# Optimization experiments

Hardware: AMD Instinct MI355X
Metric: run time of the kernel (lower is better)

The kernel has to match this reference:

```python
import jax, jax.numpy as jnp
import numpy as np

NX, NY, NZ = 432, 496, 1
D = 64        # num_pt_features
K = 3         # NUM_K
M = 1024      # memory size
BEV = 128     # num_bev_features
NCOORD = 3
NV = 10000    # pillars in scene
NP = 16384    # points in scene
BN_EPS = 1e-3
SHRINK = 0.0025


def hard_shrink_relu(x, lambd, eps=1e-12):
    return jax.nn.relu(x - lambd) * x / (jnp.abs(x - lambd) + eps)


def batchnorm_train(x, gamma, beta, eps=BN_EPS):
    # torch BatchNorm1d training-mode math (biased variance)
    mu = jnp.mean(x, axis=0)
    var = jnp.mean((x - mu) ** 2, axis=0)
    return (x - mu) * jax.lax.rsqrt(var + eps) * gamma + beta


def pdist2(a, b, eps=1e-5):
    # sqrt(eps + |  ||a||^2 + ||b||^2 - 2 a.b |), shape [n1, n2]
    n1 = jnp.sum(a * a, axis=1, keepdims=True)
    n2 = jnp.sum(b * b, axis=1, keepdims=True)
    d2 = n1 + n2.T - 2.0 * (a @ b.T)
    return jnp.sqrt(eps + jnp.abs(d2))


def memory_lookup(x_flat, mem_w, shrink):
    # MemAE-style memory unit: softmax addressing + hard shrink + L1 renorm
    att = jax.nn.softmax(x_flat @ mem_w.T, axis=1)          # [N, M]
    att = hard_shrink_relu(att, shrink)
    att = att / jnp.maximum(jnp.sum(jnp.abs(att), axis=1, keepdims=True), 1e-12)
    return att @ mem_w                                       # [N, D]


def setup_inputs() -> dict:
    key = jax.random.key(0)
    ks = jax.random.split(key, 8)
    rng = np.random.default_rng(0)
    flat = rng.choice(NX * NY, size=NV, replace=False)       # unique BEV cells
    x = (flat % NX).astype(np.int32)
    y = (flat // NX).astype(np.int32)
    coords = jnp.asarray(np.stack([np.zeros(NV, np.int32), x, y,
                                   np.zeros(NV, np.int32)], axis=1))  # (b, x, y, z)
    pc = jax.random.uniform(ks[1], (NP, 4), dtype=jnp.float32)
    point_coords = pc * jnp.array([0.0, NX, NY, 1.0], dtype=jnp.float32)
    return {
        "pillar_features": jax.random.normal(ks[0], (NV, D), dtype=jnp.float32),
        "coords": coords,
        "point_features": jax.random.normal(ks[2], (NP, D), dtype=jnp.float32),
        "point_coords": point_coords,
        "adapt_w": jax.random.normal(ks[3], (BEV // 2, D * K), dtype=jnp.float32) * 0.05,
        "bn1_g": jnp.ones((BEV // 2,), dtype=jnp.float32),
        "bn1_b": jnp.zeros((BEV // 2,), dtype=jnp.float32),
        "weight_w": jax.random.normal(ks[4], (2, BEV // 2), dtype=jnp.float32) * 0.1,
        "bn2_g": jnp.ones((2,), dtype=jnp.float32),
        "bn2_b": jnp.zeros((2,), dtype=jnp.float32),
        "mem_w": jax.random.normal(ks[5], (M, D), dtype=jnp.float32) * 0.1,
    }


def reference(pillar_features, coords, point_features, point_coords,
              adapt_w, bn1_g, bn1_b, weight_w, bn2_g, bn2_b, mem_w):
    nv = pillar_features.shape[0]
    pillars = pillar_features.T                              # [D, nv]

    # --- coord-based retrieval: smallest-K pdist(pillar coords, point coords) ---
    dist = pdist2(coords.astype(jnp.float32), point_coords)  # [nv, np]
    _, idx_c = jax.lax.top_k(-dist, K)                       # [nv, K]
    pillars_positive_coord = point_features[idx_c]           # [nv, K, D]

    # --- feature-based retrieval: top-K of softmax(points @ pillars, axis=0) ---
    score = jax.nn.softmax(point_features @ pillars, axis=0) # [np, nv]
    _, idx_f = jax.lax.top_k(score.T, K)                     # [nv, K]
    points_positive = point_features[idx_f]                  # [nv, K, D]

    # --- memory unit on both branches ---
    out_f = memory_lookup(points_positive.reshape(nv * K, D), mem_w, SHRINK).reshape(nv, K * D)
    out_c = memory_lookup(pillars_positive_coord.reshape(nv * K, D), mem_w, SHRINK).reshape(nv, K * D)

    f = jax.nn.relu(batchnorm_train(out_f @ adapt_w.T, bn1_g, bn1_b))  # [nv, 64]
    c = jax.nn.relu(batchnorm_train(out_c @ adapt_w.T, bn1_g, bn1_b))  # [nv, 64]
    w = jax.nn.softmax(batchnorm_train(pillar_features @ weight_w.T, bn2_g, bn2_b), axis=-1)
    pillars_aug = w[:, :1] * f + w[:, 1:2] * c               # [nv, 64]
    pillars_full = jnp.concatenate([pillars, pillars_aug.T], axis=0)  # [128, nv]

    # --- scatter to BEV canvas ---
    bev_idx = coords[:, 1] + coords[:, 2] * NX + coords[:, 3]
    spatial = jnp.zeros((BEV, NX * NY), dtype=pillar_features.dtype).at[:, bev_idx].set(pillars_full)
    pind = jnp.zeros((NCOORD, NX * NY), dtype=pillar_features.dtype)
    pind = pind.at[0, bev_idx].set(coords[:, 2].astype(jnp.float32))
    pind = pind.at[1, bev_idx].set(coords[:, 3].astype(jnp.float32))
    pind = pind.at[2, bev_idx].set(coords[:, 1].astype(jnp.float32))

    spatial_features = spatial.reshape(1, BEV * NZ, NY, NX)
    spatial_indices = pind.reshape(1, NCOORD * NZ, NY, NX)
    return spatial_features, spatial_indices
```

## Files before the change

### kernel.cpp

```cpp
#include <hip/hip_runtime.h>
#include <math.h>

#define NXc 432
#define NYc 496
#define NVc 10000
#define NPc 16384
#define CELLS (NXc*NYc)
#define SHRINKc 0.0025f
#define NVPAD 10048
#define NBX 27
#define NBY 31
#define NBIN (NBX*NBY)

typedef unsigned short u16;
typedef __attribute__((ext_vector_type(8))) short s16x8;
typedef __attribute__((ext_vector_type(4))) float f32x4;

__global__ void k_zero(float* __restrict__ out, int n, float* __restrict__ stats,
                       int* __restrict__ binCnt) {
    int gid = blockIdx.x * blockDim.x + threadIdx.x;
    int n4 = n >> 2;
    float4 z = make_float4(0.f, 0.f, 0.f, 0.f);
    float4* o4 = (float4*)out;
    for (int i = gid; i < n4; i += gridDim.x * blockDim.x) o4[i] = z;
    int tail = n & 3;
    if (gid < tail) out[n4 * 4 + gid] = 0.f;
    if (gid < 260) stats[gid] = 0.f;
    if (gid >= 512 && gid < 512 + NBIN) binCnt[gid - 512] = 0;
}

__device__ __forceinline__ u16 f2b(float x) {
    unsigned u = __float_as_uint(x);
    unsigned r = (u + 0x7fffu + ((u >> 16) & 1u)) >> 16;
    return (u16)r;
}
__global__ __launch_bounds__(256) void k_cast(const float* __restrict__ pillar,
                                              const float* __restrict__ pfeat,
                                              const float* __restrict__ memw,
                                              const float* __restrict__ pcoord,
                                              u16* __restrict__ pillarH,
                                              u16* __restrict__ pfeatH,
                                              u16* __restrict__ memwH,
                                              u16* __restrict__ memwTH,
                                              int* __restrict__ binCnt) {
    int idx = blockIdx.x * 256 + threadIdx.x;
    const int N1 = NVPAD * 64;
    const int N2 = N1 + NPc * 64;
    const int N3 = N2 + 65536;
    const int N4 = N3 + 65536;
    if (idx < N1) {
        int v = idx >> 6;
        pillarH[idx] = f2b(v < NVc ? pillar[idx] : 0.f);
    } else if (idx < N2) {
        int j = idx - N1;
        pfeatH[j] = f2b(pfeat[j]);
    } else if (idx < N3) {
        int j = idx - N2;
        memwH[j] = f2b(memw[j]);
    } else if (idx < N4) {
        int i = idx - N3;
        int d = i >> 10, j = i & 1023;
        memwTH[i] = f2b(memw[j * 64 + d]);
    } else {
        int j = idx - N4;
        float qx = pcoord[j * 4 + 1], qy = pcoord[j * 4 + 2];
        int bx = (int)(qx * 0.0625f); if (bx > NBX - 1) bx = NBX - 1;
        int by = (int)(qy * 0.0625f); if (by > NBY - 1) by = NBY - 1;
        atomicAdd(&binCnt[by * NBX + bx], 1);
    }
}

__global__ __launch_bounds__(1024) void k_binscan(const int* __restrict__ binCnt,
                                                  int* __restrict__ binStart,
                                                  int* __restrict__ binCursor) {
    __shared__ int sc[1024];
    int t = threadIdx.x;
    int vcount = (t < NBIN) ? binCnt[t] : 0;
    sc[t] = vcount;
    __syncthreads();
    for (int off = 1; off < 1024; off <<= 1) {
        int add = (t >= off) ? sc[t - off] : 0;
        __syncthreads();
        sc[t] += add;
        __syncthreads();
    }
    int excl = sc[t] - vcount;
    if (t <= NBIN) { binStart[t] = excl; binCursor[t] = excl; }
}

__global__ __launch_bounds__(256) void k_binfill(const float* __restrict__ pcoord,
                                                 int* __restrict__ binCursor,
                                                 float4* __restrict__ binPC) {
    int j = blockIdx.x * 256 + threadIdx.x;
    float qx = pcoord[j * 4 + 1], qy = pcoord[j * 4 + 2], qz = pcoord[j * 4 + 3];
    int bx = (int)(qx * 0.0625f); if (bx > NBX - 1) bx = NBX - 1;
    int by = (int)(qy * 0.0625f); if (by > NBY - 1) by = NBY - 1;
    int slot = atomicAdd(&binCursor[by * NBX + bx], 1);
    binPC[slot] = make_float4(qx, qy, qz * qz, __uint_as_float((unsigned)j));
}

__device__ __forceinline__ void ins_max4(unsigned &k0, unsigned &k1, unsigned &k2,
                                         unsigned &k3, unsigned t) {
    unsigned n;
    n = k0 > t ? k0 : t;  t = k0 > t ? t : k0;  k0 = n;
    n = k1 > t ? k1 : t;  t = k1 > t ? t : k1;  k1 = n;
    n = k2 > t ? k2 : t;  t = k2 > t ? t : k2;  k2 = n;
    k3 = k3 > t ? k3 : t;
}
__device__ __forceinline__ void ins_min4(unsigned &k0, unsigned &k1, unsigned &k2,
                                         unsigned &k3, unsigned t) {
    unsigned n;
    n = k0 < t ? k0 : t;  t = k0 < t ? t : k0;  k0 = n;
    n = k1 < t ? k1 : t;  t = k1 < t ? t : k1;  k1 = n;
    n = k2 < t ? k2 : t;  t = k2 < t ? t : k2;  k2 = n;
    k3 = k3 < t ? k3 : t;
}
__device__ __forceinline__ void ins_min6(unsigned kk[6], unsigned t) {
    unsigned n;
#pragma unroll
    for (int i = 0; i < 5; ++i) {
        n = kk[i] < t ? kk[i] : t;  t = kk[i] < t ? t : kk[i];  kk[i] = n;
    }
    kk[5] = kk[5] < t ? kk[5] : t;
}

__global__ __launch_bounds__(256) void k_dist6(const int* __restrict__ coords,
                                               const float4* __restrict__ binPC,
                                               const int* __restrict__ binStart,
                                               int* __restrict__ dIdx6) {
    int v = blockIdx.x * 256 + threadIdx.x;
    if (v >= NVc) return;
    int xi = coords[v * 4 + 1], yi = coords[v * 4 + 2];
    float x = (float)xi, y = (float)yi;
    int bx = xi >> 4; if (bx > NBX - 1) bx = NBX - 1;
    int by = yi >> 4; if (by > NBY - 1) by = NBY - 1;
    unsigned kk[6] = {~0u, ~0u, ~0u, ~0u, ~0u, ~0u};
    for (int r = 0; r < 32; ++r) {
        int x0 = bx - r, x1 = bx + r, y0 = by - r, y1 = by + r;
        for (int cy = y0; cy <= y1; ++cy) {
            if (cy < 0 || cy > NBY - 1) continue;
            int step = (cy == y0 || cy == y1) ? 1 : (x1 > x0 ? x1 - x0 : 1);
            for (int cx = x0; cx <= x1; cx += step) {
                if (cx < 0 || cx > NBX - 1) continue;
                int b = cy * NBX + cx;
                int s0 = binStart[b], s1 = binStart[b + 1];
                for (int s = s0; s < s1; ++s) {
                    float4 p = binPC[s];
                    float e1 = x - p.x, e2 = y - p.y;
                    float d2 = fmaf(e1, e1, fmaf(e2, e2, p.z));
                    unsigned key = (__float_as_uint(d2) & 0xFFFFC000u) | __float_as_uint(p.w);
                    ins_min6(kk, key);
                }
            }
        }
        if (kk[2] != ~0u) {
            float d3 = __uint_as_float(kk[2] & 0xFFFFC000u);
            if (256.f * (float)(r * r) > d3 * 1.004f + 1e-3f) break;
        }
    }
#pragma unroll
    for (int j = 0; j < 6; ++j) dIdx6[v * 6 + j] = (int)(kk[j] & 16383u);
}

__global__ __launch_bounds__(256) void k_score4(const u16* __restrict__ pillarH,
                                                const u16* __restrict__ pfeatH,
                                                int* __restrict__ sIdx) {
    __shared__ unsigned SH[4096];
    u16* BF = (u16*)SH;
    int t = threadIdx.x;
    int w = t >> 6, l = t & 63;
    int lm = l & 15, qd = l >> 4;
    int pb = blockIdx.x * 64;
    int cb = blockIdx.y * 1024;

    const u16* arow = pillarH + (size_t)(pb + 16 * w + lm) * 64 + qd * 8;
    s16x8 a0 = *(const s16x8*)arow;
    s16x8 a1 = *(const s16x8*)(arow + 32);

    unsigned sk[4][4];
#pragma unroll
    for (int r = 0; r < 4; ++r)
#pragma unroll
        for (int j = 0; j < 4; ++j) sk[r][j] = 0u;

    for (int s = 0; s < 8; ++s) {
        int ptb = cb + s * 128;
#pragma unroll
        for (int r = 0; r < 4; ++r) {
            int q = t + 256 * r;
            int row = q >> 3, g = q & 7;
            uint4 v = *(const uint4*)(pfeatH + (size_t)(ptb + row) * 64 + g * 8);
            *(uint4*)&BF[(((row >> 4) * 8 + g) * 16 + ((row & 15) ^ g)) * 8] = v;
        }
        __syncthreads();
#pragma unroll
        for (int pt = 0; pt < 8; ++pt) {
            s16x8 b0 = *(const s16x8*)&BF[(((pt * 8 + qd) * 16) + (lm ^ qd)) * 8];
            s16x8 b1 = *(const s16x8*)&BF[(((pt * 8 + qd + 4) * 16) + (lm ^ (qd + 4))) * 8];
            f32x4 acc = {256.f, 256.f, 256.f, 256.f};
            acc = __builtin_amdgcn_mfma_f32_16x16x32_bf16(a0, b0, acc, 0, 0, 0);
            acc = __builtin_amdgcn_mfma_f32_16x16x32_bf16(a1, b1, acc, 0, 0, 0);
            unsigned idf = (unsigned)(1023 - (s * 128 + pt * 16 + lm));
#pragma unroll
            for (int r = 0; r < 4; ++r) {
                unsigned key = (__float_as_uint(acc[r]) & 0xFFFFFC00u) | idf;
                ins_max4(sk[r][0], sk[r][1], sk[r][2], sk[r][3], key);
            }
        }
        __syncthreads();
    }
#pragma unroll
    for (int r = 0; r < 4; ++r) {
        int row = 16 * w + qd * 4 + r;
        *(uint4*)&SH[(row * 16 + lm) * 4] = make_uint4(sk[r][0], sk[r][1], sk[r][2], sk[r][3]);
    }
    __syncthreads();
    if (t < 64) {
        int gpr = pb + t;
        unsigned m0 = 0u, m1 = 0u, m2 = 0u, m3 = 0u;
#pragma unroll 4
        for (int cc = 0; cc < 16; ++cc) {
            uint4 v = *(const uint4*)&SH[(t * 16 + cc) * 4];
            ins_max4(m0, m1, m2, m3, v.x);
            ins_max4(m0, m1, m2, m3, v.y);
            ins_max4(m0, m1, m2, m3, v.z);
            ins_max4(m0, m1, m2, m3, v.w);
        }
        if (gpr < NVc) {
            int base = (blockIdx.y * NVc + gpr) * 4;
            sIdx[base + 0] = cb + 1023 - (int)(m0 & 1023u);
            sIdx[base + 1] = cb + 1023 - (int)(m1 & 1023u);
            sIdx[base + 2] = cb + 1023 - (int)(m2 & 1023u);
            sIdx[base + 3] = cb + 1023 - (int)(m3 & 1023u);
        }
    }
}

__global__ __launch_bounds__(256) void k_rerank(const float* __restrict__ pillar,
                                                const int* __restrict__ coords,
                                                const float* __restrict__ pfeat,
                                                const float* __restrict__ pcoord,
                                                const int* __restrict__ sIdx,
                                                const int* __restrict__ dIdx6,
                                                int* __restrict__ idx_f,
                                                int* __restrict__ idx_c) {
    int t = threadIdx.x;
    int wv = t >> 6, l = t & 63;
    int v = blockIdx.x * 4 + wv;
    int chunk = l >> 2, slot = l & 3;
    int ps = sIdx[(chunk * NVc + v) * 4 + slot];
    int pd = dIdx6[v * 6 + (l < 6 ? l : 0)];
    double s = 0.0;
#pragma unroll
    for (int i = 0; i < 16; ++i) {
        float4 a = *(const float4*)(pillar + v * 64 + 4 * i);
        float4 b = *(const float4*)(pfeat + ps * 64 + 4 * i);
        s += (double)a.x * (double)b.x + (double)a.y * (double)b.y
           + (double)a.z * (double)b.z + (double)a.w * (double)b.w;
    }
    float4 qc = *(const float4*)(pcoord + pd * 4);
    double db_ = (double)coords[v * 4 + 0] - (double)qc.x;
    double dx_ = (double)coords[v * 4 + 1] - (double)qc.y;
    double dy_ = (double)coords[v * 4 + 2] - (double)qc.z;
    double dz_ = (double)coords[v * 4 + 3] - (double)qc.w;
    double d2 = db_ * db_ + dx_ * dx_ + dy_ * dy_ + dz_ * dz_;
    double sv = s; int sx = ps;
    for (int k = 0; k < 3; ++k) {
        double bv = sv; int bi = sx;
#pragma unroll
        for (int off = 32; off >= 1; off >>= 1) {
            double ov = __shfl_xor(bv, off);
            int    oi = __shfl_xor(bi, off);
            if (ov > bv || (ov == bv && oi < bi)) { bv = ov; bi = oi; }
        }
        if (l == 0) idx_f[v * 3 + k] = bi;
        if (sx == bi) { sv = -INFINITY; sx = 0x7fffffff; }
    }
    double dv = d2; int dx2 = pd;
    for (int k = 0; k < 3; ++k) {
        double bv = dv; int bi = dx2;
#pragma unroll
        for (int off = 32; off >= 1; off >>= 1) {
            double ov = __shfl_xor(bv, off);
            int    oi = __shfl_xor(bi, off);
            if (ov < bv || (ov == bv && oi < bi)) { bv = ov; bi = oi; }
        }
        if (l == 0) idx_c[v * 3 + k] = bi;
        if (dx2 == bi) { dv = INFINITY; dx2 = 0x7fffffff; }
    }
}

__global__ __launch_bounds__(256) void k_mem2(const u16* __restrict__ pfeatH,
                                              const u16* __restrict__ memwH,
                                              const u16* __restrict__ memwTH,
                                              float* __restrict__ Pout) {
    __shared__ u16 WH[8192];
    __shared__ u16 WT[8192];
    __shared__ u16 ST[4][2048];
    int t = threadIdx.x;
    int w = t >> 6, l = t & 63;
    int lm = l & 15, qd = l >> 4;
    int pb = blockIdx.x * 64;

    const u16* arow = pfeatH + (size_t)(pb + 16 * w + lm) * 64 + qd * 8;
    s16x8 a0 = *(const s16x8*)arow;
    s16x8 a1 = *(const s16x8*)(arow + 32);

    float mM[4] = {-INFINITY, -INFINITY, -INFINITY, -INFINITY};
    float Zs[4] = {0.f, 0.f, 0.f, 0.f};

    for (int tile = 0; tile < 8; ++tile) {
        __syncthreads();
#pragma unroll
        for (int r = 0; r < 4; ++r) {
            int q = t + 256 * r;
            int row = q >> 3, g = q & 7;
            uint4 v = *(const uint4*)(memwH + (size_t)(tile * 128 + row) * 64 + g * 8);
            *(uint4*)&WH[(((row >> 4) * 8 + g) * 16 + ((row & 15) ^ g)) * 8] = v;
        }
        __syncthreads();
        f32x4 acc[8];
#pragma unroll
        for (int st = 0; st < 8; ++st) {
            s16x8 b0 = *(const s16x8*)&WH[((st * 8 + qd) * 16 + (lm ^ qd)) * 8];
            s16x8 b1 = *(const s16x8*)&WH[((st * 8 + qd + 4) * 16 + (lm ^ (qd + 4))) * 8];
            f32x4 z = {0.f, 0.f, 0.f, 0.f};
            z = __builtin_amdgcn_mfma_f32_16x16x32_bf16(a0, b0, z, 0, 0, 0);
            z = __builtin_amdgcn_mfma_f32_16x16x32_bf16(a1, b1, z, 0, 0, 0);
            acc[st] = z;
        }
#pragma unroll
        for (int r = 0; r < 4; ++r) {
            float tmax = acc[0][r];
#pragma unroll
            for (int st = 1; st < 8; ++st) tmax = fmaxf(tmax, acc[st][r]);
            float mn = fmaxf(mM[r], tmax);
            float zacc = Zs[r] * __expf(mM[r] - mn);
#pragma unroll
            for (int st = 0; st < 8; ++st) zacc += __expf(acc[st][r] - mn);
            mM[r] = mn; Zs[r] = zacc;
        }
    }
#pragma unroll
    for (int r = 0; r < 4; ++r) {
#pragma unroll
        for (int off = 1; off < 16; off <<= 1) {
            float om = __shfl_xor(mM[r], off);
            float oz = __shfl_xor(Zs[r], off);
            float mn = fmaxf(mM[r], om);
            Zs[r] = Zs[r] * __expf(mM[r] - mn) + oz * __expf(om - mn);
            mM[r] = mn;
        }
    }
    float invZ[4], L1[4] = {0.f, 0.f, 0.f, 0.f};
#pragma unroll
    for (int r = 0; r < 4; ++r) invZ[r] = 1.f / Zs[r];

    f32x4 oacc[4];
#pragma unroll
    for (int n = 0; n < 4; ++n) oacc[n] = (f32x4){0.f, 0.f, 0.f, 0.f};

    for (int tile = 0; tile < 8; ++tile) {
        __syncthreads();
#pragma unroll
        for (int r = 0; r < 4; ++r) {
            int q = t + 256 * r;
            int row = q >> 3, g = q & 7;
            uint4 v = *(const uint4*)(memwH + (size_t)(tile * 128 + row) * 64 + g * 8);
            *(uint4*)&WH[(((row >> 4) * 8 + g) * 16 + ((row & 15) ^ g)) * 8] = v;
        }
#pragma unroll
        for (int r = 0; r < 4; ++r) {
            int q = t + 256 * r;
            int row = q >> 4, g = q & 15;
            uint4 v = *(const uint4*)(memwTH + (size_t)row * 1024 + tile * 128 + g * 8);
            *(uint4*)&WT[(g * 64 + (row ^ g)) * 8] = v;
        }
        __syncthreads();
#pragma unroll
        for (int st = 0; st < 8; ++st) {
            s16x8 b0 = *(const s16x8*)&WH[((st * 8 + qd) * 16 + (lm ^ qd)) * 8];
            s16x8 b1 = *(const s16x8*)&WH[((st * 8 + qd + 4) * 16 + (lm ^ (qd + 4))) * 8];
            f32x4 z = {0.f, 0.f, 0.f, 0.f};
            z = __builtin_amdgcn_mfma_f32_16x16x32_bf16(a0, b0, z, 0, 0, 0);
            z = __builtin_amdgcn_mfma_f32_16x16x32_bf16(a1, b1, z, 0, 0, 0);
            int g2 = st * 2 + (lm >> 3);
#pragma unroll
            for (int r = 0; r < 4; ++r) {
                float e = __expf(z[r] - mM[r]);
                float a = e * invZ[r];
                float tt = a - SHRINKc;
                float sres = fmaxf(tt, 0.f) * a / (fabsf(tt) + 1e-12f);
                L1[r] += sres;
                int rr = qd * 4 + r;
                ST[w][(g2 * 16 + (rr ^ g2)) * 8 + (lm & 7)] = f2b(sres);
            }
        }
#pragma unroll
        for (int ks = 0; ks < 4; ++ks) {
            int g = ks * 4 + qd;
            s16x8 af = *(const s16x8*)&ST[w][(g * 16 + (lm ^ g)) * 8];
#pragma unroll
            for (int n = 0; n < 4; ++n) {
                s16x8 bf = *(const s16x8*)&WT[(g * 64 + ((n * 16 + lm) ^ g)) * 8];
                oacc[n] = __builtin_amdgcn_mfma_f32_16x16x32_bf16(af, bf, oacc[n], 0, 0, 0);
            }
        }
    }
#pragma unroll
    for (int r = 0; r < 4; ++r) {
#pragma unroll
        for (int off = 1; off < 16; off <<= 1) L1[r] += __shfl_xor(L1[r], off);
        L1[r] = 1.f / fmaxf(L1[r], 1e-12f);
    }
#pragma unroll
    for (int n = 0; n < 4; ++n)
#pragma unroll
        for (int r = 0; r < 4; ++r)
            Pout[(size_t)(pb + 16 * w + qd * 4 + r) * 64 + n * 16 + lm] = oacc[n][r] * L1[r];
}

__global__ __launch_bounds__(256) void k_proj(const float* __restrict__ Pout,
                                              const float* __restrict__ adapt,
                                              float* __restrict__ Q) {
    __shared__ float Xs[32][65];
    __shared__ float As[64][197];
    int t = threadIdx.x;
    int pb = blockIdx.x * 32;
#pragma unroll
    for (int r = 0; r < 2; ++r) {
        int q = t + 256 * r;
        int p = q >> 4, d = (q & 15) << 2;
        float4 v = *(const float4*)(Pout + (pb + p) * 64 + d);
        Xs[p][d] = v.x; Xs[p][d + 1] = v.y; Xs[p][d + 2] = v.z; Xs[p][d + 3] = v.w;
    }
#pragma unroll
    for (int r = 0; r < 12; ++r) {
        int q = t + 256 * r;
        int j = q / 48, i = (q % 48) << 2;
        float4 v = *(const float4*)(adapt + j * 192 + i);
        As[j][i] = v.x; As[j][i + 1] = v.y; As[j][i + 2] = v.z; As[j][i + 3] = v.w;
    }
    __syncthreads();
    int tr = t >> 4, tc = t & 15;
    float acc[2][12];
#pragma unroll
    for (int u = 0; u < 2; ++u)
#pragma unroll
        for (int cc = 0; cc < 12; ++cc) acc[u][cc] = 0.f;
    for (int d = 0; d < 64; ++d) {
        float xv0 = Xs[tr * 2 + 0][d];
        float xv1 = Xs[tr * 2 + 1][d];
#pragma unroll
        for (int cc = 0; cc < 12; ++cc) {
            int c = tc * 12 + cc;
            float a = As[c & 63][((c >> 6) << 6) + d];
            acc[0][cc] += xv0 * a;
            acc[1][cc] += xv1 * a;
        }
    }
#pragma unroll
    for (int u = 0; u < 2; ++u)
#pragma unroll
        for (int cc = 0; cc < 12; ++cc)
            Q[(pb + tr * 2 + u) * 192 + tc * 12 + cc] = acc[u][cc];
}

__global__ __launch_bounds__(256) void k_gather(const float* __restrict__ Q,
                                                const int* __restrict__ idx_f,
                                                const int* __restrict__ idx_c,
                                                const float* __restrict__ pillar,
                                                const float* __restrict__ ww,
                                                float* __restrict__ f_pre,
                                                float* __restrict__ c_pre,
                                                float* __restrict__ w_pre,
                                                float* __restrict__ stats) {
    __shared__ float red[4][4][64];
    __shared__ float redw[4][4];
    int t = threadIdx.x;
    int wv = t >> 6, l = t & 63;
    int base = blockIdx.x * 40;
    int vend = base + 40;
    float fs = 0, fq = 0, cs = 0, cq = 0, ws0 = 0, wq0 = 0, ws1 = 0, wq1 = 0;
    float w0l = ww[l], w1l = ww[64 + l];
    for (int v = base + wv; v < vend; v += 4) {
        int if0 = idx_f[v * 3], if1 = idx_f[v * 3 + 1], if2 = idx_f[v * 3 + 2];
        float f = Q[if0 * 192 + l] + Q[if1 * 192 + 64 + l] + Q[if2 * 192 + 128 + l];
        f_pre[v * 64 + l] = f; fs += f; fq += f * f;
        int ic0 = idx_c[v * 3], ic1 = idx_c[v * 3 + 1], ic2 = idx_c[v * 3 + 2];
        float c = Q[ic0 * 192 + l] + Q[ic1 * 192 + 64 + l] + Q[ic2 * 192 + 128 + l];
        c_pre[v * 64 + l] = c; cs += c; cq += c * c;
        float pv = pillar[v * 64 + l];
        float a0 = pv * w0l, a1 = pv * w1l;
#pragma unroll
        for (int off = 32; off >= 1; off >>= 1) {
            a0 += __shfl_xor(a0, off);
            a1 += __shfl_xor(a1, off);
        }
        if (l == 0) { w_pre[v * 2] = a0; w_pre[v * 2 + 1] = a1; }
        ws0 += a0; wq0 += a0 * a0; ws1 += a1; wq1 += a1 * a1;
    }
    red[0][wv][l] = fs; red[1][wv][l] = fq; red[2][wv][l] = cs; red[3][wv][l] = cq;
    if (l == 0) { redw[wv][0] = ws0; redw[wv][1] = wq0; redw[wv][2] = ws1; redw[wv][3] = wq1; }
    __syncthreads();
    if (wv == 0) {
#pragma unroll
        for (int q = 0; q < 4; ++q) {
            float sum = red[q][0][l] + red[q][1][l] + red[q][2][l] + red[q][3][l];
            atomicAdd(&stats[q * 64 + l], sum);
        }
        if (l < 4) {
            float sum = redw[0][l] + redw[1][l] + redw[2][l] + redw[3][l];
            atomicAdd(&stats[256 + l], sum);
        }
    }
}

__global__ __launch_bounds__(256) void k_final(const float* __restrict__ f_pre,
                                               const float* __restrict__ c_pre,
                                               const float* __restrict__ w_pre,
                                               const float* __restrict__ stats,
                                               const float* __restrict__ pillar,
                                               const int* __restrict__ coords,
                                               const float* __restrict__ g1,
                                               const float* __restrict__ b1,
                                               const float* __restrict__ g2,
                                               const float* __restrict__ b2,
                                               float* __restrict__ out) {
    int t = threadIdx.x;
    int wv = t >> 6, l = t & 63;
    int v = blockIdx.x * 4 + wv;
    const float invn = 1.0f / (float)NVc;
    float mf = stats[l] * invn;
    float vf = stats[64 + l] * invn - mf * mf;
    float rf = rsqrtf(vf + 1e-3f);
    float mc = stats[128 + l] * invn;
    float vc = stats[192 + l] * invn - mc * mc;
    float rc = rsqrtf(vc + 1e-3f);
    float mw0 = stats[256] * invn, vw0 = stats[257] * invn - mw0 * mw0;
    float mw1 = stats[258] * invn, vw1 = stats[259] * invn - mw1 * mw1;
    float rw0 = rsqrtf(vw0 + 1e-3f), rw1 = rsqrtf(vw1 + 1e-3f);
    float fb = (f_pre[v * 64 + l] - mf) * rf * g1[l] + b1[l];
    float f = fmaxf(fb, 0.f);
    float cb_ = (c_pre[v * 64 + l] - mc) * rc * g1[l] + b1[l];
    float c = fmaxf(cb_, 0.f);
    float z0 = (w_pre[v * 2] - mw0) * rw0 * g2[0] + b2[0];
    float z1 = (w_pre[v * 2 + 1] - mw1) * rw1 * g2[1] + b2[1];
    float mz = fmaxf(z0, z1);
    float e0 = __expf(z0 - mz), e1 = __expf(z1 - mz);
    float wd = 1.f / (e0 + e1);
    float aug = (e0 * wd) * f + (e1 * wd) * c;
    int cxi = coords[v * 4 + 1], cyi = coords[v * 4 + 2], czi = coords[v * 4 + 3];
    int cell = cxi + cyi * NXc + czi;
    out[l * CELLS + cell] = pillar[v * 64 + l];
    out[(64 + l) * CELLS + cell] = aug;
    if (l == 0) {
        float* o1 = out + 128 * CELLS;
        o1[cell] = (float)cyi;
        o1[CELLS + cell] = (float)czi;
        o1[2 * CELLS + cell] = (float)cxi;
    }
}

extern "C" void kernel_launch(void* const* d_in, const int* in_sizes, int n_in,
                              void* d_out, int out_size, void* d_ws, size_t ws_size,
                              hipStream_t stream) {
    const float* pillar = (const float*)d_in[0];
    const int*   coords = (const int*)d_in[1];
    const float* pfeat  = (const float*)d_in[2];
    const float* pcoord = (const float*)d_in[3];
    const float* adapt  = (const float*)d_in[4];
    const float* bn1g   = (const float*)d_in[5];
    const float* bn1b   = (const float*)d_in[6];
    const float* ww     = (const float*)d_in[7];
    const float* bn2g   = (const float*)d_in[8];
    const float* bn2b   = (const float*)d_in[9];
    const float* memw   = (const float*)d_in[10];
    float* out = (float*)d_out;
    float* ws  = (float*)d_ws;
    float* Pout  = ws + 0;
    float* Q     = ws + 1048576;
    int*   sIdx  = (int*)(ws + 4194304);
    int*   binCnt    = (int*)(ws + 4834304);
    int*   binStart  = (int*)(ws + 4835144);
    int*   binCursor = (int*)(ws + 4835984);
    int*   dIdx6     = (int*)(ws + 4836824);
    float4* binPC    = (float4*)(ws + 4896824);
    int*   idxf  = (int*)(ws + 5474304);
    int*   idxc  = (int*)(ws + 5504304);
    float* fpre  = ws + 5534304;
    float* cpre  = ws + 6174304;
    float* wpre  = ws + 6814304;
    float* stats = ws + 6834304;
    u16* pillarH = (u16*)(ws + 5534304);
    u16* pfeatH  = pillarH + (size_t)NVPAD * 64;
    u16* memwH   = (u16*)(ws + 1048576);
    u16* memwTH  = memwH + 65536;

    k_zero   <<<4096, 256, 0, stream>>>(out, out_size, stats, binCnt);
    k_cast   <<<7184, 256, 0, stream>>>(pillar, pfeat, memw, pcoord,
                                        pillarH, pfeatH, memwH, memwTH, binCnt);
    k_binscan<<<1, 1024, 0, stream>>>(binCnt, binStart, binCursor);
    k_binfill<<<64, 256, 0, stream>>>(pcoord, binCursor, binPC);
    k_score4 <<<dim3(157, 16), 256, 0, stream>>>(pillarH, pfeatH, sIdx);
    k_dist6  <<<40, 256, 0, stream>>>(coords, binPC, binStart, dIdx6);
    k_rerank <<<2500, 256, 0, stream>>>(pillar, coords, pfeat, pcoord, sIdx, dIdx6, idxf, idxc);
    k_mem2   <<<256, 256, 0, stream>>>(pfeatH, memwH, memwTH, Pout);
    k_proj   <<<512, 256, 0, stream>>>(Pout, adapt, Q);
    k_gather <<<250, 256, 0, stream>>>(Q, idxf, idxc, pillar, ww, fpre, cpre, wpre, stats);
    k_final  <<<2500, 256, 0, stream>>>(fpre, cpre, wpre, stats, pillar, coords,
                                        bn1g, bn1b, bn2g, bn2b, out);
}
```

Before: 397.7 us.

## Merge init kernels, use med3 top-k, double-buffer score tiles, MFMA projection

Merges the zero and cast kernels into one init pass and moves the bin histogram into shared-memory atomics inside the scan kernel. Top-k insertion in the distance and score kernels now uses v_med3_u32 chains instead of compare-swap sequences. The score kernel double-buffers its LDS tiles with register prefetch, which removes a barrier per stage. The fp32 projection GEMM is replaced by a bf16 MFMA kernel fed by bf16 memory-unit output and a pre-permuted bf16 adapt weight, which lowers the projection's precision.

```diff
diff --git a/kernel.cpp b/kernel.cpp
--- a/kernel.cpp
+++ b/kernel.cpp
@@ -16,17 +16,10 @@
 typedef __attribute__((ext_vector_type(8))) short s16x8;
 typedef __attribute__((ext_vector_type(4))) float f32x4;
 
-__global__ void k_zero(float* __restrict__ out, int n, float* __restrict__ stats,
-                       int* __restrict__ binCnt) {
-    int gid = blockIdx.x * blockDim.x + threadIdx.x;
-    int n4 = n >> 2;
-    float4 z = make_float4(0.f, 0.f, 0.f, 0.f);
-    float4* o4 = (float4*)out;
-    for (int i = gid; i < n4; i += gridDim.x * blockDim.x) o4[i] = z;
-    int tail = n & 3;
-    if (gid < tail) out[n4 * 4 + gid] = 0.f;
-    if (gid < 260) stats[gid] = 0.f;
-    if (gid >= 512 && gid < 512 + NBIN) binCnt[gid - 512] = 0;
+__device__ __forceinline__ unsigned med3u(unsigned a, unsigned b, unsigned c) {
+    unsigned d;
+    asm("v_med3_u32 %0, %1, %2, %3" : "=v"(d) : "v"(a), "v"(b), "v"(c));
+    return d;
 }
 
 __device__ __forceinline__ u16 f2b(float x) {
@@ -34,48 +27,63 @@
     unsigned r = (u + 0x7fffu + ((u >> 16) & 1u)) >> 16;
     return (u16)r;
 }
-__global__ __launch_bounds__(256) void k_cast(const float* __restrict__ pillar,
+
+__global__ __launch_bounds__(256) void k_init(const float* __restrict__ pillar,
                                               const float* __restrict__ pfeat,
                                               const float* __restrict__ memw,
-                                              const float* __restrict__ pcoord,
+                                              const float* __restrict__ adapt,
+                                              float* __restrict__ out, int n,
+                                              float* __restrict__ stats,
                                               u16* __restrict__ pillarH,
                                               u16* __restrict__ pfeatH,
                                               u16* __restrict__ memwH,
                                               u16* __restrict__ memwTH,
-                                              int* __restrict__ binCnt) {
-    int idx = blockIdx.x * 256 + threadIdx.x;
+                                              u16* __restrict__ badaptH) {
+    int gid = blockIdx.x * 256 + threadIdx.x;
+    float4 z = make_float4(0.f, 0.f, 0.f, 0.f);
+    float4* o4 = (float4*)out;
+    int n4 = n >> 2;
+    for (int i = gid; i < n4; i += 1835008) o4[i] = z;
+    if (gid < (n & 3)) out[n4 * 4 + gid] = 0.f;
+    if (gid < 260) stats[gid] = 0.f;
     const int N1 = NVPAD * 64;
     const int N2 = N1 + NPc * 64;
     const int N3 = N2 + 65536;
     const int N4 = N3 + 65536;
-    if (idx < N1) {
-        int v = idx >> 6;
-        pillarH[idx] = f2b(v < NVc ? pillar[idx] : 0.f);
-    } else if (idx < N2) {
-        int j = idx - N1;
-        pfeatH[j] = f2b(pfeat[j]);
-    } else if (idx < N3) {
-        int j = idx - N2;
-        memwH[j] = f2b(memw[j]);
-    } else if (idx < N4) {
-        int i = idx - N3;
+    if (gid < N1) {
+        int v = gid >> 6;
+        pillarH[gid] = f2b(v < NVc ? pillar[gid] : 0.f);
+    } else if (gid < N2) {
+        pfeatH[gid - N1] = f2b(pfeat[gid - N1]);
+    } else if (gid < N3) {
+        memwH[gid - N2] = f2b(memw[gid - N2]);
+    } else if (gid < N4) {
+        int i = gid - N3;
         int d = i >> 10, j = i & 1023;
         memwTH[i] = f2b(memw[j * 64 + d]);
     } else {
-        int j = idx - N4;
+        int i = gid - N4;
+        int c = i >> 6, d = i & 63;
+        badaptH[i] = f2b(adapt[(c & 63) * 192 + (c >> 6) * 64 + d]);
+    }
+}
+
+__global__ __launch_bounds__(1024) void k_binscan(const float* __restrict__ pcoord,
+                                                  int* __restrict__ binStart,
+                                                  int* __restrict__ binCursor) {
+    __shared__ int hcnt[1024];
+    __shared__ int sc[1024];
+    int t = threadIdx.x;
+    hcnt[t] = 0;
+    __syncthreads();
+    for (int j = t; j < NPc; j += 1024) {
         float qx = pcoord[j * 4 + 1], qy = pcoord[j * 4 + 2];
         int bx = (int)(qx * 0.0625f); if (bx > NBX - 1) bx = NBX - 1;
         int by = (int)(qy * 0.0625f); if (by > NBY - 1) by = NBY - 1;
-        atomicAdd(&binCnt[by * NBX + bx], 1);
-    }
-}
-
-__global__ __launch_bounds__(1024) void k_binscan(const int* __restrict__ binCnt,
-                                                  int* __restrict__ binStart,
-                                                  int* __restrict__ binCursor) {
-    __shared__ int sc[1024];
-    int t = threadIdx.x;
-    int vcount = (t < NBIN) ? binCnt[t] : 0;
+        atomicAdd(&hcnt[by * NBX + bx], 1);
+    }
+    __syncthreads();
+    int vcount = (t < NBIN) ? hcnt[t] : 0;
     sc[t] = vcount;
     __syncthreads();
     for (int off = 1; off < 1024; off <<= 1) {
@@ -97,31 +105,6 @@
     int by = (int)(qy * 0.0625f); if (by > NBY - 1) by = NBY - 1;
     int slot = atomicAdd(&binCursor[by * NBX + bx], 1);
     binPC[slot] = make_float4(qx, qy, qz * qz, __uint_as_float((unsigned)j));
-}
-
-__device__ __forceinline__ void ins_max4(unsigned &k0, unsigned &k1, unsigned &k2,
-                                         unsigned &k3, unsigned t) {
-    unsigned n;
-    n = k0 > t ? k0 : t;  t = k0 > t ? t : k0;  k0 = n;
-    n = k1 > t ? k1 : t;  t = k1 > t ? t : k1;  k1 = n;
-    n = k2 > t ? k2 : t;  t = k2 > t ? t : k2;  k2 = n;
-    k3 = k3 > t ? k3 : t;
-}
-__device__ __forceinline__ void ins_min4(unsigned &k0, unsigned &k1, unsigned &k2,
-                                         unsigned &k3, unsigned t) {
-    unsigned n;
-    n = k0 < t ? k0 : t;  t = k0 < t ? t : k0;  k0 = n;
-    n = k1 < t ? k1 : t;  t = k1 < t ? t : k1;  k1 = n;
-    n = k2 < t ? k2 : t;  t = k2 < t ? t : k2;  k2 = n;
-    k3 = k3 < t ? k3 : t;
-}
-__device__ __forceinline__ void ins_min6(unsigned kk[6], unsigned t) {
-    unsigned n;
-#pragma unroll
-    for (int i = 0; i < 5; ++i) {
-        n = kk[i] < t ? kk[i] : t;  t = kk[i] < t ? t : kk[i];  kk[i] = n;
-    }
-    kk[5] = kk[5] < t ? kk[5] : t;
 }
 
 __global__ __launch_bounds__(256) void k_dist6(const int* __restrict__ coords,
@@ -148,8 +131,13 @@
                     float4 p = binPC[s];
                     float e1 = x - p.x, e2 = y - p.y;
                     float d2 = fmaf(e1, e1, fmaf(e2, e2, p.z));
-                    unsigned key = (__float_as_uint(d2) & 0xFFFFC000u) | __float_as_uint(p.w);
-                    ins_min6(kk, key);
+                    unsigned t = (__float_as_uint(d2) & 0xFFFFC000u) | __float_as_uint(p.w);
+                    kk[5] = med3u(kk[4], kk[5], t);
+                    kk[4] = med3u(kk[3], kk[4], t);
+                    kk[3] = med3u(kk[2], kk[3], t);
+                    kk[2] = med3u(kk[1], kk[2], t);
+                    kk[1] = med3u(kk[0], kk[1], t);
+                    kk[0] = kk[0] < t ? kk[0] : t;
                 }
             }
         }
@@ -162,11 +150,10 @@
     for (int j = 0; j < 6; ++j) dIdx6[v * 6 + j] = (int)(kk[j] & 16383u);
 }
 
-__global__ __launch_bounds__(256) void k_score4(const u16* __restrict__ pillarH,
+__global__ __launch_bounds__(256) void k_score5(const u16* __restrict__ pillarH,
                                                 const u16* __restrict__ pfeatH,
                                                 int* __restrict__ sIdx) {
-    __shared__ unsigned SH[4096];
-    u16* BF = (u16*)SH;
+    __shared__ u16 BF[2][8192];
     int t = threadIdx.x;
     int w = t >> 6, l = t & 63;
     int lm = l & 15, qd = l >> 4;
@@ -177,6 +164,21 @@
     s16x8 a0 = *(const s16x8*)arow;
     s16x8 a1 = *(const s16x8*)(arow + 32);
 
+    int so[4], doff[4];
+#pragma unroll
+    for (int r = 0; r < 4; ++r) {
+        int q = t + 256 * r;
+        int row = q >> 3, g = q & 7;
+        so[r] = row * 64 + g * 8;
+        doff[r] = (((row >> 4) * 8 + g) * 16 + ((row & 15) ^ g)) * 8;
+    }
+    uint4 pre[4];
+    const u16* src = pfeatH + (size_t)cb * 64;
+#pragma unroll
+    for (int r = 0; r < 4; ++r) pre[r] = *(const uint4*)(src + so[r]);
+#pragma unroll
+    for (int r = 0; r < 4; ++r) *(uint4*)&BF[0][doff[r]] = pre[r];
+
     unsigned sk[4][4];
 #pragma unroll
     for (int r = 0; r < 4; ++r)
@@ -184,19 +186,17 @@
         for (int j = 0; j < 4; ++j) sk[r][j] = 0u;
 
     for (int s = 0; s < 8; ++s) {
-        int ptb = cb + s * 128;
-#pragma unroll
-        for (int r = 0; r < 4; ++r) {
-            int q = t + 256 * r;
-            int row = q >> 3, g = q & 7;
-            uint4 v = *(const uint4*)(pfeatH + (size_t)(ptb + row) * 64 + g * 8);
-            *(uint4*)&BF[(((row >> 4) * 8 + g) * 16 + ((row & 15) ^ g)) * 8] = v;
-        }
         __syncthreads();
+        if (s < 7) {
+            const u16* s2 = src + (size_t)(s + 1) * 128 * 64;
+#pragma unroll
+            for (int r = 0; r < 4; ++r) pre[r] = *(const uint4*)(s2 + so[r]);
+        }
+        const u16* B = &BF[s & 1][0];
 #pragma unroll
         for (int pt = 0; pt < 8; ++pt) {
-            s16x8 b0 = *(const s16x8*)&BF[(((pt * 8 + qd) * 16) + (lm ^ qd)) * 8];
-            s16x8 b1 = *(const s16x8*)&BF[(((pt * 8 + qd + 4) * 16) + (lm ^ (qd + 4))) * 8];
+            s16x8 b0 = *(const s16x8*)&B[(((pt * 8 + qd) * 16) + (lm ^ qd)) * 8];
+            s16x8 b1 = *(const s16x8*)&B[(((pt * 8 + qd + 4) * 16) + (lm ^ (qd + 4))) * 8];
             f32x4 acc = {256.f, 256.f, 256.f, 256.f};
             acc = __builtin_amdgcn_mfma_f32_16x16x32_bf16(a0, b0, acc, 0, 0, 0);
             acc = __builtin_amdgcn_mfma_f32_16x16x32_bf16(a1, b1, acc, 0, 0, 0);
@@ -204,15 +204,23 @@
 #pragma unroll
             for (int r = 0; r < 4; ++r) {
                 unsigned key = (__float_as_uint(acc[r]) & 0xFFFFFC00u) | idf;
-                ins_max4(sk[r][0], sk[r][1], sk[r][2], sk[r][3], key);
+                sk[r][3] = med3u(sk[r][2], sk[r][3], key);
+                sk[r][2] = med3u(sk[r][1], sk[r][2], key);
+                sk[r][1] = med3u(sk[r][0], sk[r][1], key);
+                sk[r][0] = sk[r][0] > key ? sk[r][0] : key;
             }
         }
-        __syncthreads();
-    }
+        if (s < 7) {
+#pragma unroll
+            for (int r = 0; r < 4; ++r) *(uint4*)&BF[(s + 1) & 1][doff[r]] = pre[r];
+        }
+    }
+    __syncthreads();
+    unsigned* mrg = (unsigned*)&BF[0][0];
 #pragma unroll
     for (int r = 0; r < 4; ++r) {
         int row = 16 * w + qd * 4 + r;
-        *(uint4*)&SH[(row * 16 + lm) * 4] = make_uint4(sk[r][0], sk[r][1], sk[r][2], sk[r][3]);
+        *(uint4*)&mrg[(row * 16 + lm) * 4] = make_uint4(sk[r][0], sk[r][1], sk[r][2], sk[r][3]);
     }
     __syncthreads();
     if (t < 64) {
@@ -220,11 +228,15 @@
         unsigned m0 = 0u, m1 = 0u, m2 = 0u, m3 = 0u;
 #pragma unroll 4
         for (int cc = 0; cc < 16; ++cc) {
-            uint4 v = *(const uint4*)&SH[(t * 16 + cc) * 4];
-            ins_max4(m0, m1, m2, m3, v.x);
-            ins_max4(m0, m1, m2, m3, v.y);
-            ins_max4(m0, m1, m2, m3, v.z);
-            ins_max4(m0, m1, m2, m3, v.w);
+            uint4 v = *(const uint4*)&mrg[(t * 16 + cc) * 4];
+#pragma unroll
+            for (int j = 0; j < 4; ++j) {
+                unsigned x = j == 0 ? v.x : (j == 1 ? v.y : (j == 2 ? v.z : v.w));
+                m3 = med3u(m2, m3, x);
+                m2 = med3u(m1, m2, x);
+                m1 = med3u(m0, m1, x);
+                m0 = m0 > x ? m0 : x;
+            }
         }
         if (gpr < NVc) {
             int base = (blockIdx.y * NVc + gpr) * 4;
@@ -293,7 +305,7 @@
 __global__ __launch_bounds__(256) void k_mem2(const u16* __restrict__ pfeatH,
                                               const u16* __restrict__ memwH,
                                               const u16* __restrict__ memwTH,
-                                              float* __restrict__ Pout) {
+                                              u16* __restrict__ PoutH) {
     __shared__ u16 WH[8192];
     __shared__ u16 WT[8192];
     __shared__ u16 ST[4][2048];
@@ -417,53 +429,44 @@
     for (int n = 0; n < 4; ++n)
 #pragma unroll
         for (int r = 0; r < 4; ++r)
-            Pout[(size_t)(pb + 16 * w + qd * 4 + r) * 64 + n * 16 + lm] = oacc[n][r] * L1[r];
-}
-
-__global__ __launch_bounds__(256) void k_proj(const float* __restrict__ Pout,
-                                              const float* __restrict__ adapt,
-                                              float* __restrict__ Q) {
-    __shared__ float Xs[32][65];
-    __shared__ float As[64][197];
+            PoutH[(size_t)(pb + 16 * w + qd * 4 + r) * 64 + n * 16 + lm] =
+                f2b(oacc[n][r] * L1[r]);
+}
+
+__global__ __launch_bounds__(256) void k_proj2(const u16* __restrict__ PoutH,
+                                               const u16* __restrict__ badaptH,
+                                               float* __restrict__ Q) {
+    __shared__ u16 AD[12288];
     int t = threadIdx.x;
-    int pb = blockIdx.x * 32;
-#pragma unroll
-    for (int r = 0; r < 2; ++r) {
+    int w = t >> 6, l = t & 63;
+    int lm = l & 15, qd = l >> 4;
+    int pb = blockIdx.x * 64;
+#pragma unroll
+    for (int r = 0; r < 6; ++r) {
         int q = t + 256 * r;
-        int p = q >> 4, d = (q & 15) << 2;
-        float4 v = *(const float4*)(Pout + (pb + p) * 64 + d);
-        Xs[p][d] = v.x; Xs[p][d + 1] = v.y; Xs[p][d + 2] = v.z; Xs[p][d + 3] = v.w;
-    }
-#pragma unroll
-    for (int r = 0; r < 12; ++r) {
-        int q = t + 256 * r;
-        int j = q / 48, i = (q % 48) << 2;
-        float4 v = *(const float4*)(adapt + j * 192 + i);
-        As[j][i] = v.x; As[j][i + 1] = v.y; As[j][i + 2] = v.z; As[j][i + 3] = v.w;
-    }
+        int row = q >> 3, g = q & 7;
+        uint4 v = *(const uint4*)(badaptH + (size_t)row * 64 + g * 8);
+        *(uint4*)&AD[(((row >> 4) * 8 + g) * 16 + ((row & 15) ^ g)) * 8] = v;
+    }
+    const u16* arow = PoutH + (size_t)(pb + 16 * w + lm) * 64 + qd * 8;
+    s16x8 a0 = *(const s16x8*)arow;
+    s16x8 a1 = *(const s16x8*)(arow + 32);
     __syncthreads();
-    int tr = t >> 4, tc = t & 15;
-    float acc[2][12];
-#pragma unroll
-    for (int u = 0; u < 2; ++u)
-#pragma unroll
-        for (int cc = 0; cc < 12; ++cc) acc[u][cc] = 0.f;
-    for (int d = 0; d < 64; ++d) {
-        float xv0 = Xs[tr * 2 + 0][d];
-        float xv1 = Xs[tr * 2 + 1][d];
-#pragma unroll
-        for (int cc = 0; cc < 12; ++cc) {
-            int c = tc * 12 + cc;
-            float a = As[c & 63][((c >> 6) << 6) + d];
-            acc[0][cc] += xv0 * a;
-            acc[1][cc] += xv1 * a;
-        }
-    }
-#pragma unroll
-    for (int u = 0; u < 2; ++u)
-#pragma unroll
-        for (int cc = 0; cc < 12; ++cc)
-            Q[(pb + tr * 2 + u) * 192 + tc * 12 + cc] = acc[u][cc];
+    f32x4 acc[12];
+#pragma unroll
+    for (int nt = 0; nt < 12; ++nt) {
+        s16x8 b0 = *(const s16x8*)&AD[(((nt * 8 + qd) * 16) + (lm ^ qd)) * 8];
+        s16x8 b1 = *(const s16x8*)&AD[(((nt * 8 + qd + 4) * 16) + (lm ^ (qd + 4))) * 8];
+        f32x4 z = {0.f, 0.f, 0.f, 0.f};
+        z = __builtin_amdgcn_mfma_f32_16x16x32_bf16(a0, b0, z, 0, 0, 0);
+        z = __builtin_amdgcn_mfma_f32_16x16x32_bf16(a1, b1, z, 0, 0, 0);
+        acc[nt] = z;
+    }
+#pragma unroll
+    for (int nt = 0; nt < 12; ++nt)
+#pragma unroll
+        for (int r = 0; r < 4; ++r)
+            Q[(size_t)(pb + 16 * w + qd * 4 + r) * 192 + nt * 16 + lm] = acc[nt][r];
 }
 
 __global__ __launch_bounds__(256) void k_gather(const float* __restrict__ Q,
@@ -578,14 +581,16 @@
     const float* memw   = (const float*)d_in[10];
     float* out = (float*)d_out;
     float* ws  = (float*)d_ws;
-    float* Pout  = ws + 0;
+    u16*   PoutH = (u16*)(ws + 0);
     float* Q     = ws + 1048576;
     int*   sIdx  = (int*)(ws + 4194304);
-    int*   binCnt    = (int*)(ws + 4834304);
-    int*   binStart  = (int*)(ws + 4835144);
-    int*   binCursor = (int*)(ws + 4835984);
+    int*   binStart  = (int*)(ws + 4834304);
+    int*   binCursor = (int*)(ws + 4835200);
     int*   dIdx6     = (int*)(ws + 4836824);
     float4* binPC    = (float4*)(ws + 4896824);
+    u16*   memwH   = (u16*)(ws + 4970000);
+    u16*   memwTH  = (u16*)(ws + 5002768);
+    u16*   badaptH = (u16*)(ws + 5035536);
     int*   idxf  = (int*)(ws + 5474304);
     int*   idxc  = (int*)(ws + 5504304);
     float* fpre  = ws + 5534304;
@@ -594,19 +599,16 @@
     float* stats = ws + 6834304;
     u16* pillarH = (u16*)(ws + 5534304);
     u16* pfeatH  = pillarH + (size_t)NVPAD * 64;
-    u16* memwH   = (u16*)(ws + 1048576);
-    u16* memwTH  = memwH + 65536;
-
-    k_zero   <<<4096, 256, 0, stream>>>(out, out_size, stats, binCnt);
-    k_cast   <<<7184, 256, 0, stream>>>(pillar, pfeat, memw, pcoord,
-                                        pillarH, pfeatH, memwH, memwTH, binCnt);
-    k_binscan<<<1, 1024, 0, stream>>>(binCnt, binStart, binCursor);
+
+    k_init   <<<7168, 256, 0, stream>>>(pillar, pfeat, memw, adapt, out, out_size,
+                                        stats, pillarH, pfeatH, memwH, memwTH, badaptH);
+    k_binscan<<<1, 1024, 0, stream>>>(pcoord, binStart, binCursor);
     k_binfill<<<64, 256, 0, stream>>>(pcoord, binCursor, binPC);
-    k_score4 <<<dim3(157, 16), 256, 0, stream>>>(pillarH, pfeatH, sIdx);
+    k_score5 <<<dim3(157, 16), 256, 0, stream>>>(pillarH, pfeatH, sIdx);
     k_dist6  <<<40, 256, 0, stream>>>(coords, binPC, binStart, dIdx6);
     k_rerank <<<2500, 256, 0, stream>>>(pillar, coords, pfeat, pcoord, sIdx, dIdx6, idxf, idxc);
-    k_mem2   <<<256, 256, 0, stream>>>(pfeatH, memwH, memwTH, Pout);
-    k_proj   <<<512, 256, 0, stream>>>(Pout, adapt, Q);
+    k_mem2   <<<256, 256, 0, stream>>>(pfeatH, memwH, memwTH, PoutH);
+    k_proj2  <<<256, 256, 0, stream>>>(PoutH, badaptH, Q);
     k_gather <<<250, 256, 0, stream>>>(Q, idxf, idxc, pillar, ww, fpre, cpre, wpre, stats);
     k_final  <<<2500, 256, 0, stream>>>(fpre, cpre, wpre, stats, pillar, coords,
                                         bn1g, bn1b, bn2g, bn2b, out);
```

After: 374.8 us. 1.06x faster.
